# Performance work log

Measured on AMD Instinct MI355X. Metric: run time of the kernel, lower is better.

## Reference

```python
import jax, jax.numpy as jnp
import numpy as np

B, S, D = 2, 1024, 1024
NH = 8
QK = D // 2          # qk_dim_factor = 0.5
V = D                # v_dim_factor = 1.0
DQK = QK // NH       # 64
DV = V // NH         # 128
CAP = 15.0
EPS = 1e-6


def soft_cap(t, cap=CAP):
    return cap * jnp.tanh(t / cap)


def setup_inputs() -> dict:
    key = jax.random.key(0)
    ks = jax.random.split(key, 12)
    sc = 0.02
    return {
        "x": jax.random.normal(ks[0], (B, S, D), jnp.float32),
        "Wq": jax.random.normal(ks[1], (QK, D), jnp.float32) * sc,
        "Wk": jax.random.normal(ks[2], (QK, D), jnp.float32) * sc,
        "Wv": jax.random.normal(ks[3], (V, D), jnp.float32) * sc,
        "Wog": jax.random.normal(ks[4], (V, D), jnp.float32) * sc,
        "Wi": jax.random.normal(ks[5], (NH, D), jnp.float32) * sc,
        "bi": jax.random.normal(ks[6], (NH,), jnp.float32) * sc,
        "Wf": jax.random.normal(ks[7], (NH, D), jnp.float32) * sc,
        "bf": jax.random.normal(ks[8], (NH,), jnp.float32) * sc + 3.0,  # forget-gate bias init high
        "ln_w": jnp.ones((NH * DV,), jnp.float32),
        "ln_b": jnp.zeros((NH * DV,), jnp.float32),
        "Wout": jax.random.normal(ks[9], (D, V), jnp.float32) * sc,
    }


def _mlstm_forward(x, Wq, Wk, Wv, Wog, Wi, bi, Wf, bf, ln_w, ln_b, Wout):
    Bx, Sx, _ = x.shape
    # projections
    q = (x @ Wq.T).reshape(Bx, Sx, NH, DQK)
    k = (x @ Wk.T).reshape(Bx, Sx, NH, DQK)
    v = (x @ Wv.T).reshape(Bx, Sx, NH, DV)
    o_preact = x @ Wog.T                                   # [B,S,V]
    i_pre = soft_cap(x @ Wi.T + bi)                        # [B,S,NH]
    f_pre = soft_cap(x @ Wf.T + bf)                        # [B,S,NH]

    # scan over time: move S to leading axis
    qT = jnp.moveaxis(q, 1, 0)   # [S,B,NH,DQK]
    kT = jnp.moveaxis(k, 1, 0)
    vT = jnp.moveaxis(v, 1, 0)   # [S,B,NH,DV]
    iT = jnp.moveaxis(i_pre, 1, 0)  # [S,B,NH]
    fT = jnp.moveaxis(f_pre, 1, 0)

    qk_scale = DQK ** -0.5

    def step(carry, inp):
        C, n, m = carry                       # C:[B,NH,DQK,DV] n:[B,NH,DQK] m:[B,NH]
        q_t, k_t, v_t, i_t, f_t = inp
        m_new = jnp.maximum(f_t + m, i_t)
        f_act = jnp.exp(f_t + m - m_new)      # [B,NH]
        i_act = jnp.exp(i_t - m_new)
        C = f_act[..., None, None] * C + i_act[..., None, None] * (k_t[..., :, None] * v_t[..., None, :])
        n = f_act[..., None] * n + i_act[..., None] * k_t
        qs = q_t * qk_scale
        num = jnp.einsum('bhk,bhkv->bhv', qs, C)
        qn = jnp.einsum('bhk,bhk->bh', qs, n)
        denom = jnp.maximum(jnp.abs(qn), jnp.exp(-m_new)) + 1e-6
        h_t = num / denom[..., None]          # [B,NH,DV]
        return (C, n, m_new), h_t

    C0 = jnp.zeros((Bx, NH, DQK, DV), x.dtype)
    n0 = jnp.zeros((Bx, NH, DQK), x.dtype)
    m0 = jnp.zeros((Bx, NH), x.dtype)
    _, hs = jax.lax.scan(step, (C0, n0, m0), (qT, kT, vT, iT, fT))
    h = jnp.moveaxis(hs, 0, 1).reshape(Bx, Sx, NH * DV)    # [B,S,V]

    # multi-head layer norm over flattened (NH*DV) dim
    mu = jnp.mean(h, axis=-1, keepdims=True)
    var = jnp.mean((h - mu) ** 2, axis=-1, keepdims=True)
    h_norm = (h - mu) * jax.lax.rsqrt(var + EPS) * ln_w + ln_b

    h_out = jax.nn.sigmoid(o_preact) * h_norm
    y = h_out @ Wout.T
    return y


def reference(x, Wq, Wk, Wv, Wog, Wi, bi, Wf, bf, ln_w, ln_b, Wout):
    return _mlstm_forward(x, Wq, Wk, Wv, Wog, Wi, bi, Wf, bf, ln_w, ln_b, Wout)
```

## Files before the change

kernel.cpp:

```cpp
#include <hip/hip_runtime.h>
#include <math.h>

#define SEQ  1024
#define DM   1024
#define NHD  8
#define DQKD 64
#define DVD  128
#define QKD  512
#define VD   1024
#define NB   2
#define VOC  2048

typedef __attribute__((ext_vector_type(8))) short bf16x8;
typedef __attribute__((ext_vector_type(4))) float f32x4;

__device__ __forceinline__ float softcap(float t) {
    return 15.0f * tanhf(t * (1.0f / 15.0f));
}

__device__ __forceinline__ unsigned short f2bf(float f) {
    union { float f; unsigned u; } v; v.f = f;
    unsigned r = v.u + 0x7FFFu + ((v.u >> 16) & 1u);
    return (unsigned short)(r >> 16);
}

__global__ __launch_bounds__(256) void cvt_kernel(const float* __restrict__ src,
                                                  unsigned short* __restrict__ dst, int n4) {
    int i = blockIdx.x * 256 + threadIdx.x;
    if (i < n4) {
        float4 v = ((const float4*)src)[i];
        ushort4 o;
        o.x = f2bf(v.x); o.y = f2bf(v.y); o.z = f2bf(v.z); o.w = f2bf(v.w);
        ((ushort4*)dst)[i] = o;
    }
}

__global__ __launch_bounds__(256) void gates_kernel(
    const float* __restrict__ x,
    const float* __restrict__ Wi, const float* __restrict__ bi,
    const float* __restrict__ Wf, const float* __restrict__ bf,
    float* __restrict__ ipre, float* __restrict__ fpre) {
    int wid = threadIdx.x >> 6, lane = threadIdx.x & 63;
    int row = blockIdx.x * 4 + wid;
    int b = row >> 10, t = row & 1023;
    const float* xr = x + (size_t)row * DM;
    float ai[NHD] = {}, af[NHD] = {};
    for (int d = lane; d < DM; d += 64) {
        float xv = xr[d];
#pragma unroll
        for (int h = 0; h < NHD; ++h) {
            ai[h] = fmaf(xv, Wi[h * DM + d], ai[h]);
            af[h] = fmaf(xv, Wf[h * DM + d], af[h]);
        }
    }
#pragma unroll
    for (int h = 0; h < NHD; ++h) {
        for (int off = 32; off > 0; off >>= 1) {
            ai[h] += __shfl_xor(ai[h], off);
            af[h] += __shfl_xor(af[h], off);
        }
    }
    if (lane == 0) {
#pragma unroll
        for (int h = 0; h < NHD; ++h) {
            ipre[((b * NHD + h) << 10) + t] = softcap(ai[h] + bi[h]);
            fpre[((b * NHD + h) << 10) + t] = softcap(af[h] + bf[h]);
        }
    }
}

__global__ __launch_bounds__(1024) void scan_kernel(
    const float* __restrict__ ipre, const float* __restrict__ fpre,
    float* __restrict__ gv, float* __restrict__ Mrow,
    float* __restrict__ sufg, float* __restrict__ expnegm) {
    __shared__ float sb[1024];
    int t = threadIdx.x, bh = blockIdx.x;
    int base = bh << 10;
    float f = fpre[base + t];
    sb[t] = f; __syncthreads();
    for (int off = 1; off < 1024; off <<= 1) {
        float v = sb[t];
        if (t >= off) v += sb[t - off];
        __syncthreads();
        sb[t] = v; __syncthreads();
    }
    float cumF = sb[t];
    float g = ipre[base + t] - cumF;
    gv[base + t] = g;
    __syncthreads();
    sb[t] = g; __syncthreads();
    for (int off = 1; off < 1024; off <<= 1) {
        float v = sb[t];
        if (t >= off) v = fmaxf(v, sb[t - off]);
        __syncthreads();
        sb[t] = v; __syncthreads();
    }
    float Mt = fmaxf(0.0f, sb[t]);
    Mrow[base + t] = Mt;
    expnegm[base + t] = expf(-(cumF + Mt));
    __syncthreads();
    sb[t] = g; __syncthreads();
    for (int off = 1; off < 1024; off <<= 1) {
        float v = sb[t];
        if (t + off < 1024) v = fmaxf(v, sb[t + off]);
        __syncthreads();
        sb[t] = v; __syncthreads();
    }
    sufg[base + t] = sb[t];
}

#define BM 64
#define BN 64
#define BKK 16
__global__ __launch_bounds__(256) void qk_gemm_kernel(
    const float* __restrict__ x,
    const float* __restrict__ Wq, const float* __restrict__ Wk,
    float* __restrict__ qb, float* __restrict__ kb) {
    __shared__ __align__(16) float As[BKK][BM + 4];
    __shared__ __align__(16) float Bs[BKK][BN + 4];
    int bx = blockIdx.x;
    const float* W; float* C; int col0;
    if (bx < 8) { W = Wq; C = qb; col0 = bx * BN; }
    else        { W = Wk; C = kb; col0 = (bx - 8) * BN; }
    int tid = threadIdx.x;
    int row0 = blockIdx.y * BM;
    int tx = tid & 15, ty = tid >> 4;
    int lr = tid >> 2, lc = tid & 3;
    const float* Ap = x + (size_t)(row0 + lr) * DM + lc * 4;
    const float* Bp = W + (size_t)(col0 + lr) * DM + lc * 4;
    float acc[4][4] = {};
    for (int k0 = 0; k0 < DM; k0 += BKK) {
        float4 a4 = *(const float4*)(Ap + k0);
        float4 b4 = *(const float4*)(Bp + k0);
        As[lc * 4 + 0][lr] = a4.x; As[lc * 4 + 1][lr] = a4.y;
        As[lc * 4 + 2][lr] = a4.z; As[lc * 4 + 3][lr] = a4.w;
        Bs[lc * 4 + 0][lr] = b4.x; Bs[lc * 4 + 1][lr] = b4.y;
        Bs[lc * 4 + 2][lr] = b4.z; Bs[lc * 4 + 3][lr] = b4.w;
        __syncthreads();
#pragma unroll
        for (int kk = 0; kk < BKK; ++kk) {
            float4 av = *(const float4*)(&As[kk][ty * 4]);
            float4 bv = *(const float4*)(&Bs[kk][tx * 4]);
            float ar[4] = {av.x, av.y, av.z, av.w};
            float br[4] = {bv.x, bv.y, bv.z, bv.w};
#pragma unroll
            for (int i = 0; i < 4; ++i)
#pragma unroll
                for (int j = 0; j < 4; ++j)
                    acc[i][j] = fmaf(ar[i], br[j], acc[i][j]);
        }
        __syncthreads();
    }
#pragma unroll
    for (int i = 0; i < 4; ++i) {
        float4 o4 = {acc[i][0], acc[i][1], acc[i][2], acc[i][3]};
        *(float4*)(C + (size_t)(row0 + ty * 4 + i) * QKD + col0 + tx * 4) = o4;
    }
}

__global__ __launch_bounds__(256) void mfma_nt_kernel(
    const unsigned short* __restrict__ A, const unsigned short* __restrict__ B,
    float* __restrict__ C, int ldc, int K) {
    __shared__ __align__(16) unsigned short As[128 * 32];
    __shared__ __align__(16) unsigned short Bs[128 * 32];
    int tid = threadIdx.x;
    int w = tid >> 6, l = tid & 63;
    int wr = w >> 1, wc = w & 1;
    int r0 = blockIdx.y * 128, c0 = blockIdx.x * 128;
    f32x4 acc[4][4] = {};
    for (int k0 = 0; k0 < K; k0 += 32) {
#pragma unroll
        for (int it = 0; it < 2; ++it) {
            const unsigned short* ga = A + (size_t)(r0 + it * 64 + w * 16 + (l >> 2)) * K + k0 + ((l & 3) << 3);
            __builtin_amdgcn_global_load_lds(
                (const __attribute__((address_space(1))) unsigned int*)ga,
                (__attribute__((address_space(3))) unsigned int*)&As[(it * 64 + w * 16) * 32],
                16, 0, 0);
            const unsigned short* gb = B + (size_t)(c0 + it * 64 + w * 16 + (l >> 2)) * K + k0 + ((l & 3) << 3);
            __builtin_amdgcn_global_load_lds(
                (const __attribute__((address_space(1))) unsigned int*)gb,
                (__attribute__((address_space(3))) unsigned int*)&Bs[(it * 64 + w * 16) * 32],
                16, 0, 0);
        }
        __syncthreads();
        bf16x8 af[4], bfr[4];
#pragma unroll
        for (int mi = 0; mi < 4; ++mi)
            af[mi] = *(const bf16x8*)&As[(wr * 64 + mi * 16 + (l & 15)) * 32 + ((l >> 4) << 3)];
#pragma unroll
        for (int ni = 0; ni < 4; ++ni)
            bfr[ni] = *(const bf16x8*)&Bs[(wc * 64 + ni * 16 + (l & 15)) * 32 + ((l >> 4) << 3)];
#pragma unroll
        for (int mi = 0; mi < 4; ++mi)
#pragma unroll
            for (int ni = 0; ni < 4; ++ni)
                acc[mi][ni] = __builtin_amdgcn_mfma_f32_16x16x32_bf16(af[mi], bfr[ni], acc[mi][ni], 0, 0, 0);
        __syncthreads();
    }
#pragma unroll
    for (int mi = 0; mi < 4; ++mi) {
#pragma unroll
        for (int ni = 0; ni < 4; ++ni) {
            int row = r0 + wr * 64 + mi * 16 + ((l >> 4) << 2);
            int col = c0 + wc * 64 + ni * 16 + (l & 15);
            float* cp = C + (size_t)row * ldc + col;
#pragma unroll
            for (int j = 0; j < 4; ++j) cp[(size_t)j * ldc] = acc[mi][ni][j];
        }
    }
}

__global__ __launch_bounds__(256) void attn_kernel(
    const float* __restrict__ q, const float* __restrict__ k,
    const float* __restrict__ vob, const float* __restrict__ gv,
    const float* __restrict__ Mrow, const float* __restrict__ sufg,
    const float* __restrict__ expnegm, float* __restrict__ hbuf) {
    int wid = threadIdx.x >> 6, lane = threadIdx.x & 63;
    int bh = blockIdx.x;
    int t = blockIdx.y * 4 + wid;
    int b = bh >> 3, h = bh & 7;
    int base = bh << 10;
    float Mt = Mrow[base + t];
    float qs = q[(size_t)(b * SEQ + t) * QKD + h * DQKD + lane] * 0.125f;
    float num0 = 0.0f, num1 = 0.0f, qn = 0.0f;
    for (int j = 0; j <= t; ++j) {
        if ((j & 15) == 0) {
            if (sufg[base + j] - Mt < -60.0f) break;
        }
        float kj = k[(size_t)(b * SEQ + j) * QKD + h * DQKD + lane];
        float s = qs * kj;
#pragma unroll
        for (int off = 32; off > 0; off >>= 1) s += __shfl_xor(s, off);
        float w = expf(gv[base + j] - Mt);
        float p = w * s;
        qn += p;
        const float* vr = vob + (size_t)(b * SEQ + j) * VOC + h * DVD;
        num0 = fmaf(p, vr[lane], num0);
        num1 = fmaf(p, vr[lane + 64], num1);
    }
    float denom = fmaxf(fabsf(qn), expnegm[base + t]) + 1e-6f;
    float* hr = hbuf + (size_t)(b * SEQ + t) * VD + h * DVD;
    hr[lane] = num0 / denom;
    hr[lane + 64] = num1 / denom;
}

__global__ __launch_bounds__(256) void ln_gate_kernel(
    const float* __restrict__ hbuf, const float* __restrict__ vob,
    const float* __restrict__ lnw, const float* __restrict__ lnb,
    unsigned short* __restrict__ hgbf) {
    int row = blockIdx.x, tid = threadIdx.x;
    float4 hv = ((const float4*)(hbuf + (size_t)row * VD))[tid];
    float s1 = hv.x + hv.y + hv.z + hv.w;
    float s2 = hv.x * hv.x + hv.y * hv.y + hv.z * hv.z + hv.w * hv.w;
    for (int off = 32; off > 0; off >>= 1) {
        s1 += __shfl_xor(s1, off);
        s2 += __shfl_xor(s2, off);
    }
    __shared__ float w1[4], w2[4];
    int wid = tid >> 6, lane = tid & 63;
    if (lane == 0) { w1[wid] = s1; w2[wid] = s2; }
    __syncthreads();
    s1 = w1[0] + w1[1] + w1[2] + w1[3];
    s2 = w2[0] + w2[1] + w2[2] + w2[3];
    float mean = s1 * (1.0f / 1024.0f);
    float var = s2 * (1.0f / 1024.0f) - mean * mean;
    float rs = rsqrtf(var + 1e-6f);
    float4 ov = ((const float4*)(vob + (size_t)row * VOC + VD))[tid];
    float4 wv = ((const float4*)lnw)[tid];
    float4 bv = ((const float4*)lnb)[tid];
    float ox = (1.0f / (1.0f + expf(-ov.x))) * ((hv.x - mean) * rs * wv.x + bv.x);
    float oy = (1.0f / (1.0f + expf(-ov.y))) * ((hv.y - mean) * rs * wv.y + bv.y);
    float oz = (1.0f / (1.0f + expf(-ov.z))) * ((hv.z - mean) * rs * wv.z + bv.z);
    float ow = (1.0f / (1.0f + expf(-ov.w))) * ((hv.w - mean) * rs * wv.w + bv.w);
    ushort4 o4;
    o4.x = f2bf(ox); o4.y = f2bf(oy); o4.z = f2bf(oz); o4.w = f2bf(ow);
    ((ushort4*)(hgbf + (size_t)row * VD))[tid] = o4;
}

extern "C" void kernel_launch(void* const* d_in, const int* in_sizes, int n_in,
                              void* d_out, int out_size, void* d_ws, size_t ws_size,
                              hipStream_t stream) {
    const float* x    = (const float*)d_in[0];
    const float* Wq   = (const float*)d_in[1];
    const float* Wk   = (const float*)d_in[2];
    const float* Wv   = (const float*)d_in[3];
    const float* Wog  = (const float*)d_in[4];
    const float* Wi   = (const float*)d_in[5];
    const float* bi   = (const float*)d_in[6];
    const float* Wf   = (const float*)d_in[7];
    const float* bf   = (const float*)d_in[8];
    const float* lnw  = (const float*)d_in[9];
    const float* lnb  = (const float*)d_in[10];
    const float* Wout = (const float*)d_in[11];
    float* out = (float*)d_out;

    float* ws = (float*)d_ws;
    const size_t BH   = (size_t)NB * NHD * SEQ;
    const size_t ROWS = (size_t)NB * SEQ;
    float* ipre = ws;
    float* fpre = ipre + BH;
    float* gv   = fpre + BH;
    float* Mrow = gv + BH;
    float* sufg = Mrow + BH;
    float* enm  = sufg + BH;
    float* qb   = enm + BH;
    float* kb   = qb + ROWS * QKD;
    float* vob  = kb + ROWS * QKD;
    unsigned short* xbf   = (unsigned short*)qb;
    unsigned short* Wvobf = (unsigned short*)kb;
    unsigned short* hgbf  = (unsigned short*)qb;
    unsigned short* Wobf  = (unsigned short*)kb;
    float* hb = out;

    cvt_kernel<<<2048, 256, 0, stream>>>(x, xbf, (int)(ROWS * DM / 4));
    cvt_kernel<<<1024, 256, 0, stream>>>(Wv,  Wvobf,                    VD * DM / 4);
    cvt_kernel<<<1024, 256, 0, stream>>>(Wog, Wvobf + (size_t)VD * DM,  VD * DM / 4);
    gates_kernel<<<512, 256, 0, stream>>>(x, Wi, bi, Wf, bf, ipre, fpre);
    scan_kernel<<<16, 1024, 0, stream>>>(ipre, fpre, gv, Mrow, sufg, enm);
    mfma_nt_kernel<<<dim3(VOC / 128, ROWS / 128), 256, 0, stream>>>(xbf, Wvobf, vob, VOC, DM);
    qk_gemm_kernel<<<dim3(16, ROWS / BM), 256, 0, stream>>>(x, Wq, Wk, qb, kb);
    attn_kernel<<<dim3(16, SEQ / 4), 256, 0, stream>>>(qb, kb, vob, gv, Mrow, sufg, enm, hb);
    cvt_kernel<<<1024, 256, 0, stream>>>(Wout, Wobf, DM * VD / 4);
    ln_gate_kernel<<<ROWS, 256, 0, stream>>>(hb, vob, lnw, lnb, hgbf);
    mfma_nt_kernel<<<dim3(DM / 128, ROWS / 128), 256, 0, stream>>>(hgbf, Wobf, out, DM, VD);
}
```

Baseline: 278.7 us.

## Fuse bf16 conversions, use wave-shuffle scans, and widen qk GEMM blocks

Merges the four fp32-to-bf16 conversion launches into one kernel that picks its source by block index. Workspace buffers are moved to dedicated regions so the Wout conversion no longer aliases qb/kb and can run up front. The gate scan kernel swaps its log-step shared-memory scans, each step needing two barriers, for wavefront shuffle scans plus a small cross-wave combine. The fp32 qk GEMM now uses 512 threads, with half staging A and half staging B, and each thread computes a 2x4 tile instead of 4x4. This trades per-thread work for more threads and extra workspace memory.

```diff
diff --git a/kernel.cpp b/kernel.cpp
--- a/kernel.cpp
+++ b/kernel.cpp
@@ -24,15 +24,21 @@
     return (unsigned short)(r >> 16);
 }
 
-__global__ __launch_bounds__(256) void cvt_kernel(const float* __restrict__ src,
-                                                  unsigned short* __restrict__ dst, int n4) {
-    int i = blockIdx.x * 256 + threadIdx.x;
-    if (i < n4) {
-        float4 v = ((const float4*)src)[i];
-        ushort4 o;
-        o.x = f2bf(v.x); o.y = f2bf(v.y); o.z = f2bf(v.z); o.w = f2bf(v.w);
-        ((ushort4*)dst)[i] = o;
-    }
+__global__ __launch_bounds__(256) void cvt4_kernel(
+    const float* __restrict__ s0, unsigned short* __restrict__ d0,
+    const float* __restrict__ s1, unsigned short* __restrict__ d1,
+    const float* __restrict__ s2, unsigned short* __restrict__ d2,
+    const float* __restrict__ s3, unsigned short* __restrict__ d3) {
+    int bx = blockIdx.x;
+    const float* s; unsigned short* d; int i;
+    if (bx < 2048)      { s = s0; d = d0; i = bx * 256 + threadIdx.x; }
+    else if (bx < 3072) { s = s1; d = d1; i = (bx - 2048) * 256 + threadIdx.x; }
+    else if (bx < 4096) { s = s2; d = d2; i = (bx - 3072) * 256 + threadIdx.x; }
+    else                { s = s3; d = d3; i = (bx - 4096) * 256 + threadIdx.x; }
+    float4 v = ((const float4*)s)[i];
+    ushort4 o;
+    o.x = f2bf(v.x); o.y = f2bf(v.y); o.z = f2bf(v.z); o.w = f2bf(v.w);
+    ((ushort4*)d)[i] = o;
 }
 
 __global__ __launch_bounds__(256) void gates_kernel(
@@ -73,88 +79,101 @@
     const float* __restrict__ ipre, const float* __restrict__ fpre,
     float* __restrict__ gv, float* __restrict__ Mrow,
     float* __restrict__ sufg, float* __restrict__ expnegm) {
-    __shared__ float sb[1024];
+    __shared__ float ws1[16], ws2[16], ws3[16];
     int t = threadIdx.x, bh = blockIdx.x;
     int base = bh << 10;
-    float f = fpre[base + t];
-    sb[t] = f; __syncthreads();
-    for (int off = 1; off < 1024; off <<= 1) {
-        float v = sb[t];
-        if (t >= off) v += sb[t - off];
-        __syncthreads();
-        sb[t] = v; __syncthreads();
-    }
-    float cumF = sb[t];
+    int lane = t & 63, wid = t >> 6;
+    float s = fpre[base + t];
+#pragma unroll
+    for (int off = 1; off < 64; off <<= 1) {
+        float o = __shfl_up(s, off);
+        if (lane >= off) s += o;
+    }
+    if (lane == 63) ws1[wid] = s;
+    __syncthreads();
+    float bsum = 0.0f;
+#pragma unroll
+    for (int w = 0; w < 16; ++w) { float v = ws1[w]; if (w < wid) bsum += v; }
+    float cumF = s + bsum;
     float g = ipre[base + t] - cumF;
     gv[base + t] = g;
+    float m = g;
+#pragma unroll
+    for (int off = 1; off < 64; off <<= 1) {
+        float o = __shfl_up(m, off);
+        if (lane >= off) m = fmaxf(m, o);
+    }
+    if (lane == 63) ws2[wid] = m;
     __syncthreads();
-    sb[t] = g; __syncthreads();
-    for (int off = 1; off < 1024; off <<= 1) {
-        float v = sb[t];
-        if (t >= off) v = fmaxf(v, sb[t - off]);
-        __syncthreads();
-        sb[t] = v; __syncthreads();
-    }
-    float Mt = fmaxf(0.0f, sb[t]);
+    float bmax = -1e30f;
+#pragma unroll
+    for (int w = 0; w < 16; ++w) { float v = ws2[w]; if (w < wid) bmax = fmaxf(bmax, v); }
+    float Mt = fmaxf(0.0f, fmaxf(m, bmax));
     Mrow[base + t] = Mt;
     expnegm[base + t] = expf(-(cumF + Mt));
+    float sm = g;
+#pragma unroll
+    for (int off = 1; off < 64; off <<= 1) {
+        float o = __shfl_down(sm, off);
+        if (lane + off < 64) sm = fmaxf(sm, o);
+    }
+    if (lane == 0) ws3[wid] = sm;
     __syncthreads();
-    sb[t] = g; __syncthreads();
-    for (int off = 1; off < 1024; off <<= 1) {
-        float v = sb[t];
-        if (t + off < 1024) v = fmaxf(v, sb[t + off]);
-        __syncthreads();
-        sb[t] = v; __syncthreads();
-    }
-    sufg[base + t] = sb[t];
-}
-
-#define BM 64
-#define BN 64
-#define BKK 16
-__global__ __launch_bounds__(256) void qk_gemm_kernel(
+    float amax = -1e30f;
+#pragma unroll
+    for (int w = 0; w < 16; ++w) { float v = ws3[w]; if (w > wid) amax = fmaxf(amax, v); }
+    sufg[base + t] = fmaxf(sm, amax);
+}
+
+#define QBM 64
+#define QBN 64
+#define QBK 16
+__global__ __launch_bounds__(512) void qk_gemm_kernel(
     const float* __restrict__ x,
     const float* __restrict__ Wq, const float* __restrict__ Wk,
     float* __restrict__ qb, float* __restrict__ kb) {
-    __shared__ __align__(16) float As[BKK][BM + 4];
-    __shared__ __align__(16) float Bs[BKK][BN + 4];
+    __shared__ __align__(16) float As[QBK][QBM + 4];
+    __shared__ __align__(16) float Bs[QBK][QBN + 4];
     int bx = blockIdx.x;
     const float* W; float* C; int col0;
-    if (bx < 8) { W = Wq; C = qb; col0 = bx * BN; }
-    else        { W = Wk; C = kb; col0 = (bx - 8) * BN; }
+    if (bx < 8) { W = Wq; C = qb; col0 = bx * QBN; }
+    else        { W = Wk; C = kb; col0 = (bx - 8) * QBN; }
     int tid = threadIdx.x;
-    int row0 = blockIdx.y * BM;
+    int row0 = blockIdx.y * QBM;
     int tx = tid & 15, ty = tid >> 4;
-    int lr = tid >> 2, lc = tid & 3;
-    const float* Ap = x + (size_t)(row0 + lr) * DM + lc * 4;
-    const float* Bp = W + (size_t)(col0 + lr) * DM + lc * 4;
-    float acc[4][4] = {};
-    for (int k0 = 0; k0 < DM; k0 += BKK) {
-        float4 a4 = *(const float4*)(Ap + k0);
-        float4 b4 = *(const float4*)(Bp + k0);
-        As[lc * 4 + 0][lr] = a4.x; As[lc * 4 + 1][lr] = a4.y;
-        As[lc * 4 + 2][lr] = a4.z; As[lc * 4 + 3][lr] = a4.w;
-        Bs[lc * 4 + 0][lr] = b4.x; Bs[lc * 4 + 1][lr] = b4.y;
-        Bs[lc * 4 + 2][lr] = b4.z; Bs[lc * 4 + 3][lr] = b4.w;
+    int sr = (tid & 255) >> 2, sc = tid & 3;
+    bool stageA = tid < 256;
+    const float* P = stageA ? x + (size_t)(row0 + sr) * DM + sc * 4
+                            : W + (size_t)(col0 + sr) * DM + sc * 4;
+    float acc[2][4] = {};
+    for (int k0 = 0; k0 < DM; k0 += QBK) {
+        float4 v4 = *(const float4*)(P + k0);
+        if (stageA) {
+            As[sc * 4 + 0][sr] = v4.x; As[sc * 4 + 1][sr] = v4.y;
+            As[sc * 4 + 2][sr] = v4.z; As[sc * 4 + 3][sr] = v4.w;
+        } else {
+            Bs[sc * 4 + 0][sr] = v4.x; Bs[sc * 4 + 1][sr] = v4.y;
+            Bs[sc * 4 + 2][sr] = v4.z; Bs[sc * 4 + 3][sr] = v4.w;
+        }
         __syncthreads();
 #pragma unroll
-        for (int kk = 0; kk < BKK; ++kk) {
-            float4 av = *(const float4*)(&As[kk][ty * 4]);
+        for (int kk = 0; kk < QBK; ++kk) {
+            float a0 = As[kk][ty * 2 + 0];
+            float a1 = As[kk][ty * 2 + 1];
             float4 bv = *(const float4*)(&Bs[kk][tx * 4]);
-            float ar[4] = {av.x, av.y, av.z, av.w};
             float br[4] = {bv.x, bv.y, bv.z, bv.w};
 #pragma unroll
-            for (int i = 0; i < 4; ++i)
-#pragma unroll
-                for (int j = 0; j < 4; ++j)
-                    acc[i][j] = fmaf(ar[i], br[j], acc[i][j]);
+            for (int j = 0; j < 4; ++j) {
+                acc[0][j] = fmaf(a0, br[j], acc[0][j]);
+                acc[1][j] = fmaf(a1, br[j], acc[1][j]);
+            }
         }
         __syncthreads();
     }
 #pragma unroll
-    for (int i = 0; i < 4; ++i) {
+    for (int i = 0; i < 2; ++i) {
         float4 o4 = {acc[i][0], acc[i][1], acc[i][2], acc[i][3]};
-        *(float4*)(C + (size_t)(row0 + ty * 4 + i) * QKD + col0 + tx * 4) = o4;
+        *(float4*)(C + (size_t)(row0 + ty * 2 + i) * QKD + col0 + tx * 4) = o4;
     }
 }
 
@@ -306,21 +325,21 @@
     float* qb   = enm + BH;
     float* kb   = qb + ROWS * QKD;
     float* vob  = kb + ROWS * QKD;
-    unsigned short* xbf   = (unsigned short*)qb;
-    unsigned short* Wvobf = (unsigned short*)kb;
-    unsigned short* hgbf  = (unsigned short*)qb;
-    unsigned short* Wobf  = (unsigned short*)kb;
+    unsigned short* xbf   = (unsigned short*)(vob + ROWS * VOC);
+    unsigned short* Wvobf = xbf + ROWS * DM;
+    unsigned short* Wobf  = Wvobf + (size_t)VOC * DM;
+    unsigned short* hgbf  = Wobf + (size_t)DM * VD;
     float* hb = out;
 
-    cvt_kernel<<<2048, 256, 0, stream>>>(x, xbf, (int)(ROWS * DM / 4));
-    cvt_kernel<<<1024, 256, 0, stream>>>(Wv,  Wvobf,                    VD * DM / 4);
-    cvt_kernel<<<1024, 256, 0, stream>>>(Wog, Wvobf + (size_t)VD * DM,  VD * DM / 4);
+    cvt4_kernel<<<5120, 256, 0, stream>>>(x, xbf,
+                                          Wv, Wvobf,
+                                          Wog, Wvobf + (size_t)VD * DM,
+                                          Wout, Wobf);
     gates_kernel<<<512, 256, 0, stream>>>(x, Wi, bi, Wf, bf, ipre, fpre);
     scan_kernel<<<16, 1024, 0, stream>>>(ipre, fpre, gv, Mrow, sufg, enm);
     mfma_nt_kernel<<<dim3(VOC / 128, ROWS / 128), 256, 0, stream>>>(xbf, Wvobf, vob, VOC, DM);
-    qk_gemm_kernel<<<dim3(16, ROWS / BM), 256, 0, stream>>>(x, Wq, Wk, qb, kb);
+    qk_gemm_kernel<<<dim3(16, ROWS / QBM), 512, 0, stream>>>(x, Wq, Wk, qb, kb);
     attn_kernel<<<dim3(16, SEQ / 4), 256, 0, stream>>>(qb, kb, vob, gv, Mrow, sufg, enm, hb);
-    cvt_kernel<<<1024, 256, 0, stream>>>(Wout, Wobf, DM * VD / 4);
     ln_gate_kernel<<<ROWS, 256, 0, stream>>>(hb, vob, lnw, lnb, hgbf);
     mfma_nt_kernel<<<dim3(DM / 128, ROWS / 128), 256, 0, stream>>>(hgbf, Wobf, out, DM, VD);
 }
```

Measured after the change: 293.9 us. 1.05x slower.
